# Kernel tuning notes

Hardware: AMD Instinct MI355X
Metric: run time of the kernel (lower is better)

## Reference

```python
import jax, jax.numpy as jnp
import numpy as np

H = 64                      # hidden_dim
LMAX = 3                    # hidden_lmax
DIMS = [2 * l + 1 for l in range(LMAX + 1)]   # [1, 3, 5, 7]
SIZES = [H * d for d in DIMS]                 # per-l block widths: [64, 192, 320, 448]
D_IN = sum(SIZES)                             # 1024
OUT_DIM = 128
N_ATOMS = 131072
B = 512

# e3nn normalize2mom constant for SiLU: (E_{z~N(0,1)}[silu(z)^2])^{-1/2} (~1.679)
_z = np.random.default_rng(0).standard_normal(1_000_000)
_s = _z / (1.0 + np.exp(-_z))
CST = np.float32(1.0 / np.sqrt(np.mean(_s * _s)))


def _silu(x):
    return CST * (x * jax.nn.sigmoid(x))


def setup_inputs() -> dict:
    key = jax.random.key(0)
    ks = jax.random.split(key, 16)
    inp = {
        "x": jax.random.normal(ks[0], (N_ATOMS, D_IN), dtype=jnp.float32),
        "batch_indices": jax.random.randint(ks[1], (N_ATOMS,), 0, B),
        "batch_size": B,
    }
    i = 2
    for layer in range(2):
        # l=0 path: H scalars -> H*(LMAX+1) scalars (scalars + gates); l>0: H -> H
        inp[f"W{layer}_0"] = jax.random.normal(ks[i], (H, H * (LMAX + 1)), dtype=jnp.float32); i += 1
        for l in range(1, LMAX + 1):
            inp[f"W{layer}_{l}"] = jax.random.normal(ks[i], (H, H), dtype=jnp.float32); i += 1
    inp["W_out"] = jax.random.normal(ks[i], (H, OUT_DIM), dtype=jnp.float32)
    return inp


def _layer(x, Ws):
    """e3nn Linear (block-diag per l, 1/sqrt(fan_in) norm) followed by Gate."""
    N = x.shape[0]
    parts = jnp.split(x, np.cumsum(SIZES)[:-1].tolist(), axis=1)
    norm = np.float32(1.0 / np.sqrt(H))
    y0 = (parts[0] @ Ws[0]) * norm  # (N, 4H): H scalars + 3H gates
    yl = [jnp.einsum('nmc,mo->noc', parts[l].reshape(N, H, DIMS[l]), Ws[l]) * norm
          for l in range(1, LMAX + 1)]
    s = _silu(y0[:, :H])            # activated scalars
    g = _silu(y0[:, H:])            # activated gates, (N, 3H)
    out = [s]
    for l in range(1, LMAX + 1):
        gl = g[:, (l - 1) * H:l * H]                 # (N, H)
        out.append((gl[:, :, None] * yl[l - 1]).reshape(N, H * DIMS[l]))
    return jnp.concatenate(out, axis=1)              # (N, D_IN)


def reference(x, batch_indices, batch_size, W0_0, W0_1, W0_2, W0_3,
              W1_0, W1_1, W1_2, W1_3, W_out):
    h = _layer(x, [W0_0, W0_1, W0_2, W0_3])
    h = _layer(h, [W1_0, W1_1, W1_2, W1_3])
    # dropout is identity in eval mode
    # output Linear to OUT_DIM x 0e: only the scalar (0e) block has a path
    out = (h[:, :H] @ W_out) * np.float32(1.0 / np.sqrt(H))  # (N, OUT_DIM)
    return jax.ops.segment_sum(out, batch_indices, num_segments=batch_size)
```

## Files before the change

### kernel.cpp

```cpp
#include <hip/hip_runtime.h>
#include <hip/hip_bf16.h>

#define CSTF 1.676543f
#define NREP 16

typedef __bf16 bf16x8 __attribute__((ext_vector_type(8)));
typedef float  f32x4  __attribute__((ext_vector_type(4)));

__device__ __forceinline__ float silu_n(float y) {
    return CSTF * y * __builtin_amdgcn_rcpf(1.0f + __expf(-y));
}

struct XG { f32x4 a, b, c, d; };

__device__ __forceinline__ XG loadx(const float* p) {
    XG r;
    r.a = *(const f32x4*)(p);
    r.b = *(const f32x4*)(p + 4);
    r.c = *(const f32x4*)(p + 32);
    r.d = *(const f32x4*)(p + 36);
    return r;
}

#define PROC16(cur, vb) { \
  bf16x8 a0, a1; \
  _Pragma("unroll") \
  for (int j = 0; j < 4; ++j) { \
    a0[j] = (__bf16)cur.a[j]; a0[j+4] = (__bf16)cur.b[j]; \
    a1[j] = (__bf16)cur.c[j]; a1[j+4] = (__bf16)cur.d[j]; \
  } \
  const f32x4 zf = {0.f, 0.f, 0.f, 0.f}; \
  _Pragma("unroll") \
  for (int nt = 0; nt < 4; ++nt) { \
    f32x4 acc = __builtin_amdgcn_mfma_f32_16x16x32_bf16(a0, wf0[0][nt], zf, 0, 0, 0); \
    acc = __builtin_amdgcn_mfma_f32_16x16x32_bf16(a1, wf0[1][nt], acc, 0, 0, 0); \
    _Pragma("unroll") \
    for (int r = 0; r < 4; ++r) \
      sb[w][4*g + r][nt*16 + c] = __float2bfloat16(silu_n(acc[r])); \
  } \
  const bf16x8 sa0 = *(const bf16x8*)&sb[w][c][g*8]; \
  const bf16x8 sa1 = *(const bf16x8*)&sb[w][c][g*8 + 32]; \
  _Pragma("unroll") \
  for (int nt = 0; nt < 4; ++nt) { \
    f32x4 z = __builtin_amdgcn_mfma_f32_16x16x32_bf16(sa0, wf1[0][nt], zf, 0, 0, 0); \
    z = __builtin_amdgcn_mfma_f32_16x16x32_bf16(sa1, wf1[1][nt], z, 0, 0, 0); \
    atomicAdd(&Srep[(vb.x << 6) + nt*16 + c], silu_n(z[0])); \
    atomicAdd(&Srep[(vb.y << 6) + nt*16 + c], silu_n(z[1])); \
    atomicAdd(&Srep[(vb.z << 6) + nt*16 + c], silu_n(z[2])); \
    atomicAdd(&Srep[(vb.w << 6) + nt*16 + c], silu_n(z[3])); \
  } \
}

__global__ __launch_bounds__(256, 3) void phase1(
    const float* __restrict__ x, const int* __restrict__ bidx,
    const float* __restrict__ W0, const float* __restrict__ W1,
    float* __restrict__ S)
{
    __shared__ __align__(16) __hip_bfloat16 sb[4][16][72];
    const int tid  = threadIdx.x;
    const int lane = tid & 63;
    const int w    = tid >> 6;
    const int c    = lane & 15;
    const int g    = lane >> 4;

    const int wbase = (blockIdx.x * 4 + w) * 32;
    const float* px = x + (size_t)(wbase + c) * 1024 + g * 8;

    XG c0 = loadx(px);
    XG c1 = loadx(px + 16 * 1024);
    const int4 vb0 = *(const int4*)&bidx[wbase + 4 * g];
    const int4 vb1 = *(const int4*)&bidx[wbase + 16 + 4 * g];

    bf16x8 wf0[2][4], wf1[2][4];
#pragma unroll
    for (int ks = 0; ks < 2; ++ks)
#pragma unroll
        for (int nt = 0; nt < 4; ++nt) {
            bf16x8 f0, f1;
#pragma unroll
            for (int j = 0; j < 8; ++j) {
                const int k = ks * 32 + g * 8 + j;
                f0[j] = (__bf16)(0.125f * W0[k * 256 + nt * 16 + c]);
                f1[j] = (__bf16)(0.125f * W1[k * 256 + nt * 16 + c]);
            }
            wf0[ks][nt] = f0;
            wf1[ks][nt] = f1;
        }

    float* Srep = S + ((size_t)(blockIdx.x & (NREP - 1)) << 15);

    PROC16(c0, vb0);
    PROC16(c1, vb1);
}

__global__ __launch_bounds__(128) void phase2(
    const float* __restrict__ S, const float* __restrict__ Wout,
    float* __restrict__ out)
{
    __shared__ float sp[64];
    const int b = blockIdx.x, t = threadIdx.x;
    if (t < 64) {
        float s = 0.f;
#pragma unroll
        for (int r = 0; r < NREP; ++r) s += S[((size_t)r << 15) + (b << 6) + t];
        sp[t] = s;
    }
    __syncthreads();
    float acc = 0.f;
#pragma unroll
    for (int o = 0; o < 64; ++o) acc = fmaf(sp[o], Wout[o * 128 + t], acc);
    out[b * 128 + t] = 0.125f * acc;
}

extern "C" void kernel_launch(void* const* d_in, const int* in_sizes, int n_in,
                              void* d_out, int out_size, void* d_ws, size_t ws_size,
                              hipStream_t stream)
{
    const float* x    = (const float*)d_in[0];
    const int*   bidx = (const int*)d_in[1];
    const float* W0   = (const float*)d_in[3];
    const float* W1   = (const float*)d_in[7];
    const float* Wout = (const float*)d_in[11];
    float* S   = (float*)d_ws;
    float* out = (float*)d_out;

    hipMemsetAsync(S, 0, (size_t)NREP * 32768 * sizeof(float), stream);
    hipLaunchKernelGGL(phase1, dim3(1024), dim3(256), 0, stream, x, bidx, W0, W1, S);
    hipLaunchKernelGGL(phase2, dim3(512), dim3(128), 0, stream, S, Wout, out);
}
```

Before: 49.47 us.

## Accumulate segment sums in per-block LDS table instead of global atomics

Phase1 now uses 256 blocks of 512 threads. Each block keeps a padded shared-memory table of all 512 segments by 64 channels and does its atomic adds there instead of into 16 replicated global buffers. Each wave processes 64 rows in a loop that prefetches the next 16-row group, and the block writes its partial table to the workspace at the end. This removes the memset and the contended global atomics. In exchange it uses about 139KB of LDS per block, allowing one block per CU, and phase2 must now reduce 256 partial tables instead of 16.

```diff
diff --git a/kernel.cpp b/kernel.cpp
--- a/kernel.cpp
+++ b/kernel.cpp
@@ -2,7 +2,7 @@
 #include <hip/hip_bf16.h>
 
 #define CSTF 1.676543f
-#define NREP 16
+#define TSTRIDE 68
 
 typedef __bf16 bf16x8 __attribute__((ext_vector_type(8)));
 typedef float  f32x4  __attribute__((ext_vector_type(4)));
@@ -36,40 +36,41 @@
     acc = __builtin_amdgcn_mfma_f32_16x16x32_bf16(a1, wf0[1][nt], acc, 0, 0, 0); \
     _Pragma("unroll") \
     for (int r = 0; r < 4; ++r) \
-      sb[w][4*g + r][nt*16 + c] = __float2bfloat16(silu_n(acc[r])); \
+      sbuf[w][4*g + r][nt*16 + c] = __float2bfloat16(silu_n(acc[r])); \
   } \
-  const bf16x8 sa0 = *(const bf16x8*)&sb[w][c][g*8]; \
-  const bf16x8 sa1 = *(const bf16x8*)&sb[w][c][g*8 + 32]; \
+  const bf16x8 sa0 = *(const bf16x8*)&sbuf[w][c][g*8]; \
+  const bf16x8 sa1 = *(const bf16x8*)&sbuf[w][c][g*8 + 32]; \
   _Pragma("unroll") \
   for (int nt = 0; nt < 4; ++nt) { \
     f32x4 z = __builtin_amdgcn_mfma_f32_16x16x32_bf16(sa0, wf1[0][nt], zf, 0, 0, 0); \
     z = __builtin_amdgcn_mfma_f32_16x16x32_bf16(sa1, wf1[1][nt], z, 0, 0, 0); \
-    atomicAdd(&Srep[(vb.x << 6) + nt*16 + c], silu_n(z[0])); \
-    atomicAdd(&Srep[(vb.y << 6) + nt*16 + c], silu_n(z[1])); \
-    atomicAdd(&Srep[(vb.z << 6) + nt*16 + c], silu_n(z[2])); \
-    atomicAdd(&Srep[(vb.w << 6) + nt*16 + c], silu_n(z[3])); \
+    atomicAdd(&table[vb.x * TSTRIDE + nt*16 + c], silu_n(z[0])); \
+    atomicAdd(&table[vb.y * TSTRIDE + nt*16 + c], silu_n(z[1])); \
+    atomicAdd(&table[vb.z * TSTRIDE + nt*16 + c], silu_n(z[2])); \
+    atomicAdd(&table[vb.w * TSTRIDE + nt*16 + c], silu_n(z[3])); \
   } \
 }
 
-__global__ __launch_bounds__(256, 3) void phase1(
+__global__ __launch_bounds__(512, 1) void phase1(
     const float* __restrict__ x, const int* __restrict__ bidx,
     const float* __restrict__ W0, const float* __restrict__ W1,
-    float* __restrict__ S)
+    float* __restrict__ ws)
 {
-    __shared__ __align__(16) __hip_bfloat16 sb[4][16][72];
+    __shared__ float table[512 * TSTRIDE];
+    __shared__ __align__(16) __hip_bfloat16 sbuf[8][16][72];
     const int tid  = threadIdx.x;
     const int lane = tid & 63;
     const int w    = tid >> 6;
     const int c    = lane & 15;
     const int g    = lane >> 4;
 
-    const int wbase = (blockIdx.x * 4 + w) * 32;
+    const int wbase = (blockIdx.x * 8 + w) * 64;
     const float* px = x + (size_t)(wbase + c) * 1024 + g * 8;
 
-    XG c0 = loadx(px);
-    XG c1 = loadx(px + 16 * 1024);
-    const int4 vb0 = *(const int4*)&bidx[wbase + 4 * g];
-    const int4 vb1 = *(const int4*)&bidx[wbase + 16 + 4 * g];
+    XG   cc = loadx(px);
+    int4 bb = *(const int4*)&bidx[wbase + 4 * g];
+
+    for (int i = tid; i < 512 * TSTRIDE; i += 512) table[i] = 0.0f;
 
     bf16x8 wf0[2][4], wf1[2][4];
 #pragma unroll
@@ -86,29 +87,50 @@
             wf0[ks][nt] = f0;
             wf1[ks][nt] = f1;
         }
+    __syncthreads();
 
-    float* Srep = S + ((size_t)(blockIdx.x & (NREP - 1)) << 15);
+#pragma unroll 1
+    for (int gi = 0; gi < 4; ++gi) {
+        XG   nc = cc;
+        int4 nb = bb;
+        if (gi < 3) {
+            nc = loadx(px + (size_t)(gi + 1) * 16 * 1024);
+            nb = *(const int4*)&bidx[wbase + (gi + 1) * 16 + 4 * g];
+        }
+        PROC16(cc, bb);
+        cc = nc;
+        bb = nb;
+    }
+    __syncthreads();
 
-    PROC16(c0, vb0);
-    PROC16(c1, vb1);
+    float* dst = ws + (size_t)blockIdx.x * 32768;
+    for (int j = tid; j < 8192; j += 512) {
+        const int b  = j >> 4;
+        const int o4 = (j & 15) * 4;
+        *(f32x4*)&dst[b * 64 + o4] = *(const f32x4*)&table[b * TSTRIDE + o4];
+    }
 }
 
 __global__ __launch_bounds__(128) void phase2(
-    const float* __restrict__ S, const float* __restrict__ Wout,
+    const float* __restrict__ ws, const float* __restrict__ Wout,
     float* __restrict__ out)
 {
-    __shared__ float sp[64];
+    __shared__ float sp[128];
     const int b = blockIdx.x, t = threadIdx.x;
-    if (t < 64) {
-        float s = 0.f;
-#pragma unroll
-        for (int r = 0; r < NREP; ++r) s += S[((size_t)r << 15) + (b << 6) + t];
-        sp[t] = s;
-    }
+    const int o = t & 63, half = t >> 6;
+
+    float s = 0.f;
+    for (int blk = half; blk < 256; blk += 2)
+        s += ws[(size_t)blk * 32768 + b * 64 + o];
+    sp[t] = s;
     __syncthreads();
+
     float acc = 0.f;
 #pragma unroll
-    for (int o = 0; o < 64; ++o) acc = fmaf(sp[o], Wout[o * 128 + t], acc);
+    for (int o2 = 0; o2 < 64; ++o2) {
+        const float S = sp[o2] + sp[o2 + 64];
+        acc = fmaf(S, Wout[o2 * 128 + t], acc);
+    }
     out[b * 128 + t] = 0.125f * acc;
 }
 
@@ -121,10 +143,9 @@
     const float* W0   = (const float*)d_in[3];
     const float* W1   = (const float*)d_in[7];
     const float* Wout = (const float*)d_in[11];
-    float* S   = (float*)d_ws;
+    float* ws  = (float*)d_ws;
     float* out = (float*)d_out;
 
-    hipMemsetAsync(S, 0, (size_t)NREP * 32768 * sizeof(float), stream);
-    hipLaunchKernelGGL(phase1, dim3(1024), dim3(256), 0, stream, x, bidx, W0, W1, S);
-    hipLaunchKernelGGL(phase2, dim3(512), dim3(128), 0, stream, S, Wout, out);
+    hipLaunchKernelGGL(phase1, dim3(256), dim3(512), 0, stream, x, bidx, W0, W1, ws);
+    hipLaunchKernelGGL(phase2, dim3(512), dim3(128), 0, stream, ws, Wout, out);
 }
```

Measured after the change: 92.59 us. +87.2%, slower.
